# Optimization experiments

Measured on AMD Instinct MI355X. Metric: run time of the kernel, lower is better.

The kernel has to match this reference:

```python
import math
import jax, jax.numpy as jnp
import numpy as np

FIRE_THRESH = 0.85
_C = math.sqrt(2.0 / math.pi)

def _normalize(v, axis=-1, eps=1e-12):
    # matches torch F.normalize: v / max(||v||, eps)
    n = jnp.linalg.norm(v, axis=axis, keepdims=True)
    return v / jnp.maximum(n, eps)

def setup_inputs() -> dict:
    key = jax.random.key(0)
    k1, k2, k3 = jax.random.split(key, 3)
    B, T, D, N = 8, 4096, 1024, 512
    x = jax.random.normal(k1, (B, T, D), dtype=jnp.float32)
    buf = jax.random.normal(k2, (N, D), dtype=jnp.float32)
    depl = jax.random.uniform(k3, (N,), dtype=jnp.float32)
    mask = jnp.ones((N,), dtype=bool)
    ptr = 3  # static ring-buffer write position
    log_k = jnp.asarray(math.log(2.0), dtype=jnp.float32)
    logit_depl_rate = jnp.asarray(0.0, dtype=jnp.float32)
    logit_floor = jnp.asarray(math.log(0.1 / 0.9), dtype=jnp.float32)
    return {"x": x, "buf": buf, "depl": depl, "mask": mask, "ptr": ptr,
            "log_k": log_k, "logit_depl_rate": logit_depl_rate, "logit_floor": logit_floor}

def reference(x, buf, depl, mask, ptr, log_k, logit_depl_rate, logit_floor):
    # steady-state (_ready=True) forward of GELU244
    k_gate = jnp.clip(jnp.exp(log_k), 0.1, 8.0)
    depl_rate = 0.1 + 0.8 * jax.nn.sigmoid(logit_depl_rate)
    floor_val = 0.5 * jax.nn.sigmoid(logit_floor)
    # tanh-approx GELU
    y = 0.5 * x * (1.0 + jnp.tanh(_C * (x + 0.044715 * x ** 3)))  # [B,T,D]
    D = x.shape[-1]
    m_curr = jax.lax.stop_gradient(jnp.mean(y.reshape(-1, D), axis=0))  # [D]
    m_n = _normalize(m_curr, axis=0)  # unit vector [D]
    buf_n = _normalize(buf, axis=-1)  # [N,D]
    sims = jnp.where(mask, buf_n @ m_n, -1.0)  # [N]
    idx = jnp.argmax(sims)
    max_sim = sims[idx]
    depl_level = depl[idx]
    # .item() in torch => no grad through k_gate / depl_level here
    raw_gate = jnp.exp(-jax.lax.stop_gradient(k_gate) * (1.0 - jax.lax.stop_gradient(depl_level)))
    gate = floor_val + (1.0 - floor_val) * raw_gate
    output = y * gate
    # no_grad state update: deplete fired slot, write m_n at ring pointer
    factor = jnp.where(max_sim > FIRE_THRESH, jax.lax.stop_gradient(depl_rate), 1.0)
    new_depl = depl.at[idx].multiply(factor)
    new_buf = buf.at[ptr].set(m_n)
    new_depl = new_depl.at[ptr].set(1.0)
    new_mask = mask.at[ptr].set(True)
    return output, new_buf, new_depl, new_mask
```

## Files before the change

kernel.cpp:

```cpp
#include <hip/hip_runtime.h>
#include <math.h>

#define D_DIM   1024
#define D4      256
#define A_BLOCKS 1024

#define GELU_C 0.7978845608028654f

__device__ __forceinline__ float gelu_tanh(float x) {
    float x3 = x * x * x;
    float a  = GELU_C * __builtin_fmaf(0.044715f, x3, x);
    return x / (1.0f + __expf(-2.0f * a));
}

__global__ __launch_bounds__(256) void colsum_partial(
        const float* __restrict__ x, float* __restrict__ partial,
        int rows, int rows_per_block) {
    int t = threadIdx.x;
    int b = blockIdx.x;
    const float4* x4 = (const float4*)x;
    float4 acc = make_float4(0.f, 0.f, 0.f, 0.f);
    int r0 = b * rows_per_block;
    int r1 = min(r0 + rows_per_block, rows);
    #pragma unroll 4
    for (int r = r0; r < r1; ++r) {
        float4 v = x4[(size_t)r * D4 + t];
        acc.x += gelu_tanh(v.x);
        acc.y += gelu_tanh(v.y);
        acc.z += gelu_tanh(v.z);
        acc.w += gelu_tanh(v.w);
    }
    ((float4*)partial)[(size_t)b * D4 + t] = acc;
}

__global__ __launch_bounds__(256) void reduce_partial(
        const float* __restrict__ partial, float* __restrict__ partial2) {
    int cg = blockIdx.x & 3;
    int pg = blockIdx.x >> 2;
    int c  = cg * 256 + threadIdx.x;
    float s = 0.f;
    int p0 = pg * (A_BLOCKS / 8);
    #pragma unroll 4
    for (int p = p0; p < p0 + A_BLOCKS / 8; ++p)
        s += partial[(size_t)p * D_DIM + c];
    partial2[pg * D_DIM + c] = s;
}

__global__ __launch_bounds__(1024) void finalize_mn(
        const float* __restrict__ partial2, float* __restrict__ m_n,
        float* __restrict__ out_buf, const int* __restrict__ ptr_p,
        float inv_rows) {
    int c = threadIdx.x;
    float s = 0.f;
    #pragma unroll
    for (int pg = 0; pg < 8; ++pg) s += partial2[pg * D_DIM + c];
    float m = s * inv_rows;
    float sq = m * m;
    #pragma unroll
    for (int off = 32; off > 0; off >>= 1) sq += __shfl_down(sq, off, 64);
    __shared__ float red[16];
    int wid = c >> 6, lane = c & 63;
    if (lane == 0) red[wid] = sq;
    __syncthreads();
    __shared__ float snorm;
    if (c == 0) {
        float tot = 0.f;
        #pragma unroll
        for (int i = 0; i < 16; ++i) tot += red[i];
        snorm = fmaxf(sqrtf(tot), 1e-12f);
    }
    __syncthreads();
    float v = m / snorm;
    m_n[c] = v;
    out_buf[(size_t)ptr_p[0] * D_DIM + c] = v;
}

__global__ __launch_bounds__(256) void sims_and_copy(
        const float* __restrict__ buf, const float* __restrict__ m_n,
        float* __restrict__ sims, float* __restrict__ out_buf,
        const int* __restrict__ ptr_p) {
    int n = blockIdx.x, t = threadIdx.x;
    float4 v = ((const float4*)(buf + (size_t)n * D_DIM))[t];
    float4 w = ((const float4*)m_n)[t];
    float dot = v.x*w.x + v.y*w.y + v.z*w.z + v.w*w.w;
    float sq  = v.x*v.x + v.y*v.y + v.z*v.z + v.w*v.w;
    #pragma unroll
    for (int off = 32; off > 0; off >>= 1) {
        dot += __shfl_down(dot, off, 64);
        sq  += __shfl_down(sq,  off, 64);
    }
    __shared__ float rd[4], rs[4];
    int wid = t >> 6, lane = t & 63;
    if (lane == 0) { rd[wid] = dot; rs[wid] = sq; }
    __syncthreads();
    if (t == 0) {
        float dd = rd[0] + rd[1] + rd[2] + rd[3];
        float ss = rs[0] + rs[1] + rs[2] + rs[3];
        sims[n] = dd / fmaxf(sqrtf(ss), 1e-12f);
    }
    if (n != ptr_p[0])
        ((float4*)(out_buf + (size_t)n * D_DIM))[t] = v;
}

__global__ __launch_bounds__(512) void gate_and_state(
        const float* __restrict__ sims, const float* __restrict__ depl,
        const float* __restrict__ log_k, const float* __restrict__ logit_depl_rate,
        const float* __restrict__ logit_floor, const int* __restrict__ ptr_p,
        float* __restrict__ gate_out, float* __restrict__ out_depl,
        float* __restrict__ out_mask, int N) {
    __shared__ float sval[512];
    __shared__ int   sidx[512];
    int t = threadIdx.x;
    sval[t] = (t < N) ? sims[t] : -INFINITY;
    sidx[t] = t;
    __syncthreads();
    for (int s = 256; s > 0; s >>= 1) {
        if (t < s) {
            float a = sval[t], b = sval[t + s];
            int ia = sidx[t], ib = sidx[t + s];
            if (b > a || (b == a && ib < ia)) { sval[t] = b; sidx[t] = ib; }
        }
        __syncthreads();
    }
    __shared__ float sfac;
    __shared__ int   sIdx;
    if (t == 0) {
        int idx = sidx[0];
        float max_sim = sval[0];
        float k_gate    = fminf(fmaxf(__expf(log_k[0]), 0.1f), 8.0f);
        float depl_rate = 0.1f + 0.8f / (1.0f + __expf(-logit_depl_rate[0]));
        float floor_val = 0.5f / (1.0f + __expf(-logit_floor[0]));
        float raw_gate  = __expf(-k_gate * (1.0f - depl[idx]));
        gate_out[0] = floor_val + (1.0f - floor_val) * raw_gate;
        sfac = (max_sim > 0.85f) ? depl_rate : 1.0f;
        sIdx = idx;
    }
    __syncthreads();
    if (t < N) {
        float nd = depl[t] * (t == sIdx ? sfac : 1.0f);
        if (t == ptr_p[0]) nd = 1.0f;
        out_depl[t] = nd;
        out_mask[t] = 1.0f;
    }
}

__global__ __launch_bounds__(256) void gelu_gate_out(
        const float* __restrict__ x, const float* __restrict__ gate_p,
        float* __restrict__ out, int n4) {
    float gate = gate_p[0];
    int stride = gridDim.x * blockDim.x;
    const float4* x4 = (const float4*)x;
    float4* o4 = (float4*)out;
    for (int i = blockIdx.x * blockDim.x + threadIdx.x; i < n4; i += stride) {
        float4 v = x4[i];
        float4 r;
        r.x = gelu_tanh(v.x) * gate;
        r.y = gelu_tanh(v.y) * gate;
        r.z = gelu_tanh(v.z) * gate;
        r.w = gelu_tanh(v.w) * gate;
        o4[i] = r;
    }
}

extern "C" void kernel_launch(void* const* d_in, const int* in_sizes, int n_in,
                              void* d_out, int out_size, void* d_ws, size_t ws_size,
                              hipStream_t stream) {
    const float* x     = (const float*)d_in[0];
    const float* buf   = (const float*)d_in[1];
    const float* depl  = (const float*)d_in[2];
    const int*   ptr_p = (const int*)d_in[4];
    const float* log_k = (const float*)d_in[5];
    const float* ldr   = (const float*)d_in[6];
    const float* lf    = (const float*)d_in[7];

    int xN   = in_sizes[0];
    int bufN = in_sizes[1];
    int N    = in_sizes[2];
    int rows = xN / D_DIM;

    float* out      = (float*)d_out;
    float* out_buf  = out + xN;
    float* out_depl = out_buf + bufN;
    float* out_mask = out_depl + N;

    float* ws       = (float*)d_ws;
    float* partial2 = ws;
    float* m_n      = ws + 8 * D_DIM;
    float* sims     = m_n + D_DIM;
    float* gate     = sims + N;
    float* partial  = out;

    int rpb = (rows + A_BLOCKS - 1) / A_BLOCKS;

    hipLaunchKernelGGL(colsum_partial, dim3(A_BLOCKS), dim3(256), 0, stream,
                       x, partial, rows, rpb);
    hipLaunchKernelGGL(reduce_partial, dim3(32), dim3(256), 0, stream,
                       partial, partial2);
    hipLaunchKernelGGL(finalize_mn, dim3(1), dim3(1024), 0, stream,
                       partial2, m_n, out_buf, ptr_p, 1.0f / (float)rows);
    hipLaunchKernelGGL(sims_and_copy, dim3(N), dim3(256), 0, stream,
                       buf, m_n, sims, out_buf, ptr_p);
    hipLaunchKernelGGL(gate_and_state, dim3(1), dim3(512), 0, stream,
                       sims, depl, log_k, ldr, lf, ptr_p, gate, out_depl, out_mask, N);
    hipLaunchKernelGGL(gelu_gate_out, dim3(2048), dim3(256), 0, stream,
                       x, gate, out, xN / 4);
}
```

Baseline: 92.89 us.

## Merge reduction and normalization stages and simplify GELU arithmetic

Removes the single-block finalize kernel by having the column-reduce kernel produce the unnormalized column sum directly. The norm is computed by an extra block in the similarity kernel, and the normalization is deferred into the argmax/state kernel, which also writes the ring-buffer row. It also rewrites the tanh-GELU with pre-folded constants and a hardware reciprocal, moves partials from the output buffer to workspace, and unrolls the output loop. The launch count drops by one, at the cost of slight numeric differences from the approximate reciprocal and the reordered normalization.

```diff
diff --git a/kernel.cpp b/kernel.cpp
--- a/kernel.cpp
+++ b/kernel.cpp
@@ -1,16 +1,18 @@
 #include <hip/hip_runtime.h>
 #include <math.h>
 
-#define D_DIM   1024
-#define D4      256
+#define D_DIM    1024
+#define D4       256
 #define A_BLOCKS 1024
-
-#define GELU_C 0.7978845608028654f
+#define N_SLOTS  512
+
+#define GK1 0.07135481627f
+#define GK2 1.59576912161f
 
 __device__ __forceinline__ float gelu_tanh(float x) {
-    float x3 = x * x * x;
-    float a  = GELU_C * __builtin_fmaf(0.044715f, x3, x);
-    return x / (1.0f + __expf(-2.0f * a));
+    float t = x * __builtin_fmaf(GK1, x * x, GK2);
+    float e = __expf(-t);
+    return x * __builtin_amdgcn_rcpf(1.0f + e);
 }
 
 __global__ __launch_bounds__(256) void colsum_partial(
@@ -33,55 +35,48 @@
     ((float4*)partial)[(size_t)b * D4 + t] = acc;
 }
 
-__global__ __launch_bounds__(256) void reduce_partial(
-        const float* __restrict__ partial, float* __restrict__ partial2) {
-    int cg = blockIdx.x & 3;
-    int pg = blockIdx.x >> 2;
-    int c  = cg * 256 + threadIdx.x;
+__global__ __launch_bounds__(256) void reduce_cols(
+        const float* __restrict__ partial, float* __restrict__ s_out) {
+    __shared__ float red[8][32];
+    int t  = threadIdx.x, b = blockIdx.x;
+    int cl = t & 31, sl = t >> 5;
+    int c  = b * 32 + cl;
     float s = 0.f;
-    int p0 = pg * (A_BLOCKS / 8);
+    int p0 = sl * (A_BLOCKS / 8);
     #pragma unroll 4
     for (int p = p0; p < p0 + A_BLOCKS / 8; ++p)
         s += partial[(size_t)p * D_DIM + c];
-    partial2[pg * D_DIM + c] = s;
-}
-
-__global__ __launch_bounds__(1024) void finalize_mn(
-        const float* __restrict__ partial2, float* __restrict__ m_n,
-        float* __restrict__ out_buf, const int* __restrict__ ptr_p,
-        float inv_rows) {
-    int c = threadIdx.x;
-    float s = 0.f;
-    #pragma unroll
-    for (int pg = 0; pg < 8; ++pg) s += partial2[pg * D_DIM + c];
-    float m = s * inv_rows;
-    float sq = m * m;
-    #pragma unroll
-    for (int off = 32; off > 0; off >>= 1) sq += __shfl_down(sq, off, 64);
-    __shared__ float red[16];
-    int wid = c >> 6, lane = c & 63;
-    if (lane == 0) red[wid] = sq;
-    __syncthreads();
-    __shared__ float snorm;
-    if (c == 0) {
+    red[sl][cl] = s;
+    __syncthreads();
+    if (t < 32) {
         float tot = 0.f;
         #pragma unroll
-        for (int i = 0; i < 16; ++i) tot += red[i];
-        snorm = fmaxf(sqrtf(tot), 1e-12f);
-    }
-    __syncthreads();
-    float v = m / snorm;
-    m_n[c] = v;
-    out_buf[(size_t)ptr_p[0] * D_DIM + c] = v;
-}
-
-__global__ __launch_bounds__(256) void sims_and_copy(
-        const float* __restrict__ buf, const float* __restrict__ m_n,
-        float* __restrict__ sims, float* __restrict__ out_buf,
-        const int* __restrict__ ptr_p) {
+        for (int i = 0; i < 8; ++i) tot += red[i][t];
+        s_out[b * 32 + t] = tot;
+    }
+}
+
+__global__ __launch_bounds__(256) void sims_norm(
+        const float* __restrict__ buf, const float* __restrict__ s_vec,
+        float* __restrict__ snorm_out, float* __restrict__ dotraw,
+        float* __restrict__ out_buf, const int* __restrict__ ptr_p,
+        float eps_s) {
     int n = blockIdx.x, t = threadIdx.x;
+    int wid = t >> 6, lane = t & 63;
+    if (n == N_SLOTS) {
+        float4 w = ((const float4*)s_vec)[t];
+        float sq = w.x*w.x + w.y*w.y + w.z*w.z + w.w*w.w;
+        #pragma unroll
+        for (int off = 32; off > 0; off >>= 1) sq += __shfl_down(sq, off, 64);
+        __shared__ float rs[4];
+        if (lane == 0) rs[wid] = sq;
+        __syncthreads();
+        if (t == 0)
+            snorm_out[0] = fmaxf(sqrtf(rs[0] + rs[1] + rs[2] + rs[3]), eps_s);
+        return;
+    }
     float4 v = ((const float4*)(buf + (size_t)n * D_DIM))[t];
-    float4 w = ((const float4*)m_n)[t];
+    float4 w = ((const float4*)s_vec)[t];
     float dot = v.x*w.x + v.y*w.y + v.z*w.z + v.w*w.w;
     float sq  = v.x*v.x + v.y*v.y + v.z*v.z + v.w*v.w;
     #pragma unroll
@@ -89,29 +84,29 @@
         dot += __shfl_down(dot, off, 64);
         sq  += __shfl_down(sq,  off, 64);
     }
-    __shared__ float rd[4], rs[4];
-    int wid = t >> 6, lane = t & 63;
-    if (lane == 0) { rd[wid] = dot; rs[wid] = sq; }
+    __shared__ float rd[4], rs2[4];
+    if (lane == 0) { rd[wid] = dot; rs2[wid] = sq; }
     __syncthreads();
     if (t == 0) {
         float dd = rd[0] + rd[1] + rd[2] + rd[3];
-        float ss = rs[0] + rs[1] + rs[2] + rs[3];
-        sims[n] = dd / fmaxf(sqrtf(ss), 1e-12f);
+        float ss = rs2[0] + rs2[1] + rs2[2] + rs2[3];
+        dotraw[n] = dd / fmaxf(sqrtf(ss), 1e-12f);
     }
     if (n != ptr_p[0])
         ((float4*)(out_buf + (size_t)n * D_DIM))[t] = v;
 }
 
-__global__ __launch_bounds__(512) void gate_and_state(
-        const float* __restrict__ sims, const float* __restrict__ depl,
+__global__ __launch_bounds__(512) void gate_state(
+        const float* __restrict__ dotraw, const float* __restrict__ snorm_p,
+        const float* __restrict__ s_vec, const float* __restrict__ depl,
         const float* __restrict__ log_k, const float* __restrict__ logit_depl_rate,
         const float* __restrict__ logit_floor, const int* __restrict__ ptr_p,
         float* __restrict__ gate_out, float* __restrict__ out_depl,
-        float* __restrict__ out_mask, int N) {
+        float* __restrict__ out_mask, float* __restrict__ out_buf) {
     __shared__ float sval[512];
     __shared__ int   sidx[512];
     int t = threadIdx.x;
-    sval[t] = (t < N) ? sims[t] : -INFINITY;
+    sval[t] = dotraw[t];
     sidx[t] = t;
     __syncthreads();
     for (int s = 256; s > 0; s >>= 1) {
@@ -124,9 +119,10 @@
     }
     __shared__ float sfac;
     __shared__ int   sIdx;
+    float snorm = snorm_p[0];
     if (t == 0) {
         int idx = sidx[0];
-        float max_sim = sval[0];
+        float max_sim = sval[0] / snorm;
         float k_gate    = fminf(fmaxf(__expf(log_k[0]), 0.1f), 8.0f);
         float depl_rate = 0.1f + 0.8f / (1.0f + __expf(-logit_depl_rate[0]));
         float floor_val = 0.5f / (1.0f + __expf(-logit_floor[0]));
@@ -136,12 +132,13 @@
         sIdx = idx;
     }
     __syncthreads();
-    if (t < N) {
-        float nd = depl[t] * (t == sIdx ? sfac : 1.0f);
-        if (t == ptr_p[0]) nd = 1.0f;
-        out_depl[t] = nd;
-        out_mask[t] = 1.0f;
-    }
+    int ptr = ptr_p[0];
+    float nd = depl[t] * (t == sIdx ? sfac : 1.0f);
+    if (t == ptr) nd = 1.0f;
+    out_depl[t] = nd;
+    out_mask[t] = 1.0f;
+    out_buf[(size_t)ptr * D_DIM + t]       = s_vec[t]       / snorm;
+    out_buf[(size_t)ptr * D_DIM + t + 512] = s_vec[t + 512] / snorm;
 }
 
 __global__ __launch_bounds__(256) void gelu_gate_out(
@@ -151,6 +148,7 @@
     int stride = gridDim.x * blockDim.x;
     const float4* x4 = (const float4*)x;
     float4* o4 = (float4*)out;
+    #pragma unroll 4
     for (int i = blockIdx.x * blockDim.x + threadIdx.x; i < n4; i += stride) {
         float4 v = x4[i];
         float4 r;
@@ -175,33 +173,32 @@
 
     int xN   = in_sizes[0];
     int bufN = in_sizes[1];
-    int N    = in_sizes[2];
     int rows = xN / D_DIM;
 
     float* out      = (float*)d_out;
     float* out_buf  = out + xN;
     float* out_depl = out_buf + bufN;
-    float* out_mask = out_depl + N;
-
-    float* ws       = (float*)d_ws;
-    float* partial2 = ws;
-    float* m_n      = ws + 8 * D_DIM;
-    float* sims     = m_n + D_DIM;
-    float* gate     = sims + N;
-    float* partial  = out;
+    float* out_mask = out_depl + N_SLOTS;
+
+    float* ws      = (float*)d_ws;
+    float* s_vec   = ws;
+    float* snorm   = ws + 1024;
+    float* gate    = ws + 1025;
+    float* dotraw  = ws + 1040;
+    float* partial = ws + 2048;
 
     int rpb = (rows + A_BLOCKS - 1) / A_BLOCKS;
+    float eps_s = 1e-12f * (float)rows;
 
     hipLaunchKernelGGL(colsum_partial, dim3(A_BLOCKS), dim3(256), 0, stream,
                        x, partial, rows, rpb);
-    hipLaunchKernelGGL(reduce_partial, dim3(32), dim3(256), 0, stream,
-                       partial, partial2);
-    hipLaunchKernelGGL(finalize_mn, dim3(1), dim3(1024), 0, stream,
-                       partial2, m_n, out_buf, ptr_p, 1.0f / (float)rows);
-    hipLaunchKernelGGL(sims_and_copy, dim3(N), dim3(256), 0, stream,
-                       buf, m_n, sims, out_buf, ptr_p);
-    hipLaunchKernelGGL(gate_and_state, dim3(1), dim3(512), 0, stream,
-                       sims, depl, log_k, ldr, lf, ptr_p, gate, out_depl, out_mask, N);
+    hipLaunchKernelGGL(reduce_cols, dim3(32), dim3(256), 0, stream,
+                       partial, s_vec);
+    hipLaunchKernelGGL(sims_norm, dim3(N_SLOTS + 1), dim3(256), 0, stream,
+                       buf, s_vec, snorm, dotraw, out_buf, ptr_p, eps_s);
+    hipLaunchKernelGGL(gate_state, dim3(1), dim3(512), 0, stream,
+                       dotraw, snorm, s_vec, depl, log_k, ldr, lf, ptr_p,
+                       gate, out_depl, out_mask, out_buf);
     hipLaunchKernelGGL(gelu_gate_out, dim3(2048), dim3(256), 0, stream,
                        x, gate, out, xN / 4);
 }
```

After: 86.91 us. 1.07x faster.
